# Kernel optimization log

Measured on AMD Instinct MI355X. Metric: run time of the kernel, lower is better.

Reference implementation:

```python
import jax, jax.numpy as jnp
import numpy as np

D = 256          # d_model
NH = 8           # n_heads
HD = D // NH
LEV = 3          # n_levels
NP = 4           # n_points
DFF = 1024       # d_ffn
B = 8            # batch
LQ = 3600        # 60*60 queries (hardcoded in get_reference_points)
SHAPES = np.array([[60, 60], [30, 30], [15, 15]], dtype=np.int64)
LIN = int((SHAPES[:, 0] * SHAPES[:, 1]).sum())  # 4725
START = np.concatenate([[0], np.cumsum(SHAPES[:, 0] * SHAPES[:, 1])[:-1]]).astype(np.int64)


def setup_inputs() -> dict:
    key = jax.random.key(0)
    ks = iter(jax.random.split(key, 32))
    def lin(k, o, i):
        return jax.random.normal(k, (o, i), jnp.float32) * 0.02
    return {
        "tgt": jax.random.normal(next(ks), (LQ, B, D), jnp.float32),
        "query_pos": jax.random.normal(next(ks), (1, 1, D), jnp.float32),
        "src": jax.random.normal(next(ks), (B, LIN, D), jnp.float32),
        "src_spatial_shapes": jnp.asarray(SHAPES),
        "level_start_index": jnp.asarray(START),
        "in_proj_w": lin(next(ks), 3 * D, D),
        "in_proj_b": jnp.zeros((3 * D,), jnp.float32),
        "out_proj_w": lin(next(ks), D, D),
        "out_proj_b": jnp.zeros((D,), jnp.float32),
        "samp_off_w": lin(next(ks), NH * LEV * NP * 2, D),
        "samp_off_b": jax.random.normal(next(ks), (NH * LEV * NP * 2,), jnp.float32) * 0.5,
        "attn_w_w": lin(next(ks), NH * LEV * NP, D),
        "attn_w_b": jnp.zeros((NH * LEV * NP,), jnp.float32),
        "value_proj_w": lin(next(ks), D, D),
        "value_proj_b": jnp.zeros((D,), jnp.float32),
        "cross_out_w": lin(next(ks), D, D),
        "cross_out_b": jnp.zeros((D,), jnp.float32),
        "ln1_g": jnp.ones((D,), jnp.float32), "ln1_b": jnp.zeros((D,), jnp.float32),
        "ln2_g": jnp.ones((D,), jnp.float32), "ln2_b": jnp.zeros((D,), jnp.float32),
        "ln3_g": jnp.ones((D,), jnp.float32), "ln3_b": jnp.zeros((D,), jnp.float32),
        "ffn_w1": lin(next(ks), DFF, D), "ffn_b1": jnp.zeros((DFF,), jnp.float32),
        "ffn_w2": lin(next(ks), D, DFF), "ffn_b2": jnp.zeros((D,), jnp.float32),
    }


def _ln(x, g, b, eps=1e-5):
    m = x.mean(-1, keepdims=True)
    v = ((x - m) ** 2).mean(-1, keepdims=True)
    return (x - m) * jax.lax.rsqrt(v + eps) * g + b


def _self_attn(q_in, k_in, v_in, wqkv, bqkv, wo, bo):
    # torch nn.MultiheadAttention semantics, inputs laid out (seq, batch, embed)
    S, N, _ = q_in.shape
    q = (q_in @ wqkv[:D].T + bqkv[:D]).reshape(S, N, NH, HD)
    k = (k_in @ wqkv[D:2 * D].T + bqkv[D:2 * D]).reshape(S, N, NH, HD)
    v = (v_in @ wqkv[2 * D:].T + bqkv[2 * D:]).reshape(S, N, NH, HD)
    logits = jnp.einsum('snhd,tnhd->nhst', q, k) / np.sqrt(HD).astype(np.float32)
    a = jax.nn.softmax(logits, -1)
    ctx = jnp.einsum('nhst,tnhd->snhd', a, v).reshape(S, N, D)
    return ctx @ wo.T + bo


def _bilinear(v_l, loc, Hl, Wl):
    # v_l: [B, NH, Hl*Wl, HD]; loc: [B, NH, LQ, NP, 2] normalized in [0,1]
    # grid_sample(align_corners=False, padding=zeros): pixel = loc*size - 0.5
    x = loc[..., 0] * Wl - 0.5
    y = loc[..., 1] * Hl - 0.5
    x0 = jnp.floor(x); y0 = jnp.floor(y)
    fx = x - x0; fy = y - y0
    x0 = x0.astype(jnp.int32); y0 = y0.astype(jnp.int32)
    def corner(yi, xi, w):
        valid = ((xi >= 0) & (xi < Wl) & (yi >= 0) & (yi < Hl)).astype(v_l.dtype)
        idx = jnp.clip(yi, 0, Hl - 1) * Wl + jnp.clip(xi, 0, Wl - 1)
        b, h, lq, p = idx.shape
        g = jnp.take_along_axis(v_l, idx.reshape(b, h, lq * p)[..., None], axis=2)
        return g.reshape(b, h, lq, p, HD) * (w * valid)[..., None]
    return (corner(y0, x0, (1 - fx) * (1 - fy))
            + corner(y0, x0 + 1, fx * (1 - fy))
            + corner(y0 + 1, x0, (1 - fx) * fy)
            + corner(y0 + 1, x0 + 1, fx * fy))


def _msdeform(query, ref, src, wso, bso, waw, baw, wv, bv, wo, bo):
    Bq, Lq, _ = query.shape
    value = (src @ wv.T + bv).reshape(Bq, LIN, NH, HD).transpose(0, 2, 1, 3)  # [B,NH,LIN,HD]
    off = (query @ wso.T + bso).reshape(Bq, Lq, NH, LEV, NP, 2)
    aw = (query @ waw.T + baw).reshape(Bq, Lq, NH, LEV * NP)
    aw = jax.nn.softmax(aw, -1).reshape(Bq, Lq, NH, LEV, NP)
    normalizer = jnp.asarray(SHAPES[:, ::-1].copy(), jnp.float32)  # (W, H) per level
    loc = ref[:, :, None, :, None, :] + off / normalizer[None, None, None, :, None, :]
    out = jnp.zeros((Bq, NH, Lq, HD), query.dtype)
    for l in range(LEV):
        Hl, Wl = int(SHAPES[l, 0]), int(SHAPES[l, 1])
        s = int(START[l])
        v_l = value[:, :, s:s + Hl * Wl]
        loc_l = loc[:, :, :, l].transpose(0, 2, 1, 3, 4)      # [B,NH,LQ,NP,2]
        sampled = _bilinear(v_l, loc_l, Hl, Wl)               # [B,NH,LQ,NP,HD]
        out = out + (sampled * aw[:, :, :, l].transpose(0, 2, 1, 3)[..., None]).sum(3)
    out = out.transpose(0, 2, 1, 3).reshape(Bq, Lq, D)
    return out @ wo.T + bo


def _reference_points():
    Hh = Ww = 60
    ys = (jnp.arange(Hh, dtype=jnp.float32) + 0.5) / Hh
    xs = (jnp.arange(Ww, dtype=jnp.float32) + 0.5) / Ww
    yy, xx = jnp.meshgrid(ys, xs, indexing='ij')
    ref = jnp.stack([xx.reshape(-1), yy.reshape(-1)], -1)[None]  # [1, 3600, 2]
    return jnp.broadcast_to(ref[:, :, None, :], (1, Hh * Ww, LEV, 2))


def reference(tgt, query_pos, src, src_spatial_shapes, level_start_index,
              in_proj_w, in_proj_b, out_proj_w, out_proj_b,
              samp_off_w, samp_off_b, attn_w_w, attn_w_b,
              value_proj_w, value_proj_b, cross_out_w, cross_out_b,
              ln1_g, ln1_b, ln2_g, ln2_b, ln3_g, ln3_b,
              ffn_w1, ffn_b1, ffn_w2, ffn_b2):
    # dropout layers are identity (eval mode). spatial shapes are static metadata
    # (SHAPES/START) since slicing sizes must be static under jit.
    q = (tgt + query_pos).transpose(1, 0, 2)
    tgt2 = _self_attn(q, q, tgt.transpose(1, 0, 2), in_proj_w, in_proj_b, out_proj_w, out_proj_b)
    t = _ln(tgt + tgt2.transpose(1, 0, 2), ln2_g, ln2_b)
    ref = _reference_points()
    tq = t.transpose(1, 0, 2)  # permute(1,0,2) -> [B, LQ, D]
    tgt2 = _msdeform(tq + query_pos, ref, src, samp_off_w, samp_off_b,
                     attn_w_w, attn_w_b, value_proj_w, value_proj_b,
                     cross_out_w, cross_out_b)
    tq = _ln(tq + tgt2, ln1_g, ln1_b)
    ff = jax.nn.relu(tq @ ffn_w1.T + ffn_b1) @ ffn_w2.T + ffn_b2
    tq = _ln(tq + ff, ln3_g, ln3_b)
    return tq.transpose(1, 0, 2)  # [LQ, B, D]
```

## Files before the change

kernel.cpp:

```cpp
#include <hip/hip_runtime.h>
#include <hip/hip_bf16.h>
#include <cstddef>
#include <cstdint>

#define D_MODEL 256
#define NHEAD   8
#define HDIM    32
#define NLEV    3
#define NPNT    4
#define DFF     1024
#define BATCH   8
#define LQ      3600
#define LIN     4725
#define MROWS   (BATCH*LQ)

typedef short bf16x8 __attribute__((ext_vector_type(8)));
typedef float f32x4  __attribute__((ext_vector_type(4)));

__device__ __forceinline__ unsigned short f2b(float x) {
    unsigned int u = __float_as_uint(x);
    unsigned int r = (u + 0x7fffu + ((u >> 16) & 1u)) >> 16;
    return (unsigned short)r;
}
__device__ __forceinline__ float b2f(unsigned short s) {
    return __uint_as_float(((unsigned int)s) << 16);
}

#define GLDS16(g, l) __builtin_amdgcn_global_load_lds( \
    (const __attribute__((address_space(1))) void*)(g), \
    (__attribute__((address_space(3))) void*)(l), 16, 0, 0)

#define WTOT 991232
__global__ __launch_bounds__(256) void prep_kernel(
    const float* __restrict__ tgt, unsigned short* __restrict__ tgtb,
    const float* __restrict__ srcf, unsigned short* __restrict__ srcb,
    const float* __restrict__ w_in, const float* __restrict__ w_out,
    const float* __restrict__ w_val, const float* __restrict__ w_cross,
    const float* __restrict__ w_so, const float* __restrict__ w_aw,
    const float* __restrict__ w_f1, const float* __restrict__ w_f2,
    unsigned short* __restrict__ wdst,
    const float* __restrict__ qp, const float* __restrict__ so_b,
    const float* __restrict__ aw_b, float* __restrict__ qpv)
{
    const int bid = blockIdx.x;
    const int tid = threadIdx.x;
    if (bid < 7200) {
        int i = bid * 256 + tid;
        float4 v = ((const float4*)tgt)[i];
        ushort4 o; o.x = f2b(v.x); o.y = f2b(v.y); o.z = f2b(v.z); o.w = f2b(v.w);
        ((ushort4*)tgtb)[i] = o;
    } else if (bid < 16650) {
        int i = (bid - 7200) * 256 + tid;
        float4 v = ((const float4*)srcf)[i];
        ushort4 o; o.x = f2b(v.x); o.y = f2b(v.y); o.z = f2b(v.z); o.w = f2b(v.w);
        ((ushort4*)srcb)[i] = o;
    } else if (bid < 17618) {
        int idx = ((bid - 16650) * 256 + tid) * 4;
        if (idx >= WTOT) return;
        const float* src; int off;
        if      (idx < 196608) { src = w_in;    off = idx; }
        else if (idx < 262144) { src = w_out;   off = idx - 196608; }
        else if (idx < 327680) { src = w_val;   off = idx - 262144; }
        else if (idx < 393216) { src = w_cross; off = idx - 327680; }
        else if (idx < 442368) { src = w_so;    off = idx - 393216; }
        else if (idx < 466944) { src = w_aw;    off = idx - 442368; }
        else if (idx < 729088) { src = w_f1;    off = idx - 466944; }
        else                   { src = w_f2;    off = idx - 729088; }
        float4 v = *(const float4*)(src + off);
        ushort4 o; o.x = f2b(v.x); o.y = f2b(v.y); o.z = f2b(v.z); o.w = f2b(v.w);
        *(ushort4*)(wdst + idx) = o;
    } else {
        int o = (bid - 17618) * 256 + tid;
        if (o >= 768 + 192 + 96) return;
        const float* wrow;
        if (o < 768)       wrow = w_in + (size_t)o * D_MODEL;
        else if (o < 960)  wrow = w_so + (size_t)(o - 768) * D_MODEL;
        else               wrow = w_aw + (size_t)(o - 960) * D_MODEL;
        float acc = 0.f;
        for (int d = 0; d < D_MODEL; ++d) acc += qp[d] * wrow[d];
        qpv[o] = acc;
        if (o >= 768) {
            float bias = (o < 960) ? so_b[o - 768] : aw_b[o - 960];
            qpv[1056 + (o - 768)] = acc + bias;
        }
    }
}

__global__ __launch_bounds__(256) void gemm_bf16(
    const unsigned short* __restrict__ A,
    const unsigned short* __restrict__ W,
    const float* __restrict__ bias,
    const float* __restrict__ bias2, int b2lim,
    float* __restrict__ Cf, unsigned short* __restrict__ Cb,
    int M, int N, int K, int relu)
{
    __shared__ __align__(16) unsigned short As[2 * 128 * 32];
    __shared__ __align__(16) unsigned short Bs[2 * 128 * 32];
    const int tid  = threadIdx.x;
    const int wave = tid >> 6;
    const int lane = tid & 63;
    const int m0 = blockIdx.x * 128;
    const int n0 = blockIdx.y * 128;

    const int lr  = lane >> 2;
    const int lc8 = (lane & 3) * 8;
    int ar0 = m0 + wave * 32 + lr;      if (ar0 > M - 1) ar0 = M - 1;
    int ar1 = m0 + wave * 32 + 16 + lr; if (ar1 > M - 1) ar1 = M - 1;
    int br0 = n0 + wave * 32 + lr;      if (br0 > N - 1) br0 = N - 1;
    int br1 = n0 + wave * 32 + 16 + lr; if (br1 > N - 1) br1 = N - 1;
    const unsigned short* pa0 = A + (size_t)ar0 * K + lc8;
    const unsigned short* pa1 = A + (size_t)ar1 * K + lc8;
    const unsigned short* pb0 = W + (size_t)br0 * K + lc8;
    const unsigned short* pb1 = W + (size_t)br1 * K + lc8;
    unsigned short* la0 = As + wave * 1024;
    unsigned short* la1 = As + wave * 1024 + 512;
    unsigned short* lb0 = Bs + wave * 1024;
    unsigned short* lb1 = Bs + wave * 1024 + 512;

    const int wm = (wave >> 1) * 64;
    const int wn = (wave & 1) * 64;
    const int fr = lane & 15;
    const int fk = (lane >> 4) * 8;

    f32x4 acc[4][4] = {};

    for (int k0 = 0; k0 < K; k0 += 64) {
        GLDS16(pa0, la0); GLDS16(pa0 + 32, la0 + 4096);
        GLDS16(pa1, la1); GLDS16(pa1 + 32, la1 + 4096);
        GLDS16(pb0, lb0); GLDS16(pb0 + 32, lb0 + 4096);
        GLDS16(pb1, lb1); GLDS16(pb1 + 32, lb1 + 4096);
        pa0 += 64; pa1 += 64; pb0 += 64; pb1 += 64;
        __syncthreads();
#pragma unroll
        for (int p = 0; p < 2; ++p) {
            bf16x8 af[4], bfv[4];
#pragma unroll
            for (int i = 0; i < 4; ++i)
                af[i] = *(const bf16x8*)&As[p * 4096 + (wm + i * 16 + fr) * 32 + fk];
#pragma unroll
            for (int j = 0; j < 4; ++j)
                bfv[j] = *(const bf16x8*)&Bs[p * 4096 + (wn + j * 16 + fr) * 32 + fk];
#pragma unroll
            for (int i = 0; i < 4; ++i)
#pragma unroll
                for (int j = 0; j < 4; ++j)
                    acc[i][j] = __builtin_amdgcn_mfma_f32_16x16x32_bf16(
                        af[i], bfv[j], acc[i][j], 0, 0, 0);
        }
        __syncthreads();
    }

    const int quad = lane >> 4;
#pragma unroll
    for (int j = 0; j < 4; ++j) {
        const int col = n0 + wn + j * 16 + fr;
        if (col >= N) continue;
        float bv = 0.f;
        if (bias) bv += bias[col];
        if (bias2 && col < b2lim) bv += bias2[col];
#pragma unroll
        for (int i = 0; i < 4; ++i) {
#pragma unroll
            for (int r = 0; r < 4; ++r) {
                const int row = m0 + wm + i * 16 + quad * 4 + r;
                if (row >= M) continue;
                float v = acc[i][j][r] + bv;
                if (relu) v = fmaxf(v, 0.f);
                if (Cf) Cf[(size_t)row * N + col] = v;
                if (Cb) Cb[(size_t)row * N + col] = f2b(v);
            }
        }
    }
}

__global__ __launch_bounds__(256) void gemm_ln(
    const unsigned short* __restrict__ A,
    const unsigned short* __restrict__ W,
    const float* __restrict__ bias,
    const float* __restrict__ resid,
    const float* __restrict__ g, const float* __restrict__ bb,
    float* __restrict__ outf, unsigned short* __restrict__ outb, int K)
{
    __shared__ __align__(16) unsigned short As[2 * 64 * 32];
    __shared__ __align__(16) unsigned short Bs[2 * 256 * 32];
    const int tid  = threadIdx.x;
    const int wave = tid >> 6;
    const int lane = tid & 63;
    const int m0 = blockIdx.x * 64;

    const int arow = tid >> 2;
    const int akc  = (tid & 3) * 8;
    const unsigned short* pa = A + (size_t)(m0 + arow) * K + akc;
    unsigned short* la = As + tid * 8;
    const unsigned short* pb0 = W + (size_t)(arow)       * K + akc;
    const unsigned short* pb1 = W + (size_t)(64  + arow) * K + akc;
    const unsigned short* pb2 = W + (size_t)(128 + arow) * K + akc;
    const unsigned short* pb3 = W + (size_t)(192 + arow) * K + akc;
    unsigned short* lb0 = Bs + tid * 8;
    unsigned short* lb1 = Bs + 2048 + tid * 8;
    unsigned short* lb2 = Bs + 4096 + tid * 8;
    unsigned short* lb3 = Bs + 6144 + tid * 8;

    const int fr = lane & 15;
    const int fk = (lane >> 4) * 8;
    const int quad = lane >> 4;
    const int colbase = wave * 64;

    f32x4 acc[4][4] = {};

    for (int k0 = 0; k0 < K; k0 += 64) {
        GLDS16(pa, la);        GLDS16(pa + 32, la + 2048);
        GLDS16(pb0, lb0);      GLDS16(pb0 + 32, lb0 + 8192);
        GLDS16(pb1, lb1);      GLDS16(pb1 + 32, lb1 + 8192);
        GLDS16(pb2, lb2);      GLDS16(pb2 + 32, lb2 + 8192);
        GLDS16(pb3, lb3);      GLDS16(pb3 + 32, lb3 + 8192);
        pa += 64; pb0 += 64; pb1 += 64; pb2 += 64; pb3 += 64;
        __syncthreads();
#pragma unroll
        for (int p = 0; p < 2; ++p) {
            bf16x8 af[4], bfv[4];
#pragma unroll
            for (int i = 0; i < 4; ++i)
                af[i] = *(const bf16x8*)&As[p * 2048 + (i * 16 + fr) * 32 + fk];
#pragma unroll
            for (int j = 0; j < 4; ++j)
                bfv[j] = *(const bf16x8*)&Bs[p * 8192 + (colbase + j * 16 + fr) * 32 + fk];
#pragma unroll
            for (int i = 0; i < 4; ++i)
#pragma unroll
                for (int j = 0; j < 4; ++j)
                    acc[i][j] = __builtin_amdgcn_mfma_f32_16x16x32_bf16(
                        af[i], bfv[j], acc[i][j], 0, 0, 0);
        }
        __syncthreads();
    }

    float2* red = (float2*)As;
    float rs[4][4], rq[4][4];
#pragma unroll
    for (int i = 0; i < 4; ++i) {
#pragma unroll
        for (int r = 0; r < 4; ++r) {
            const int row = m0 + i * 16 + quad * 4 + r;
            float s = 0.f, q = 0.f;
#pragma unroll
            for (int j = 0; j < 4; ++j) {
                const int col = colbase + j * 16 + fr;
                float v = acc[i][j][r] + bias[col] + resid[(size_t)row * 256 + col];
                acc[i][j][r] = v;
                s += v; q += v * v;
            }
            rs[i][r] = s; rq[i][r] = q;
        }
    }
#pragma unroll
    for (int off = 1; off < 16; off <<= 1) {
#pragma unroll
        for (int i = 0; i < 4; ++i)
#pragma unroll
            for (int r = 0; r < 4; ++r) {
                rs[i][r] += __shfl_xor(rs[i][r], off);
                rq[i][r] += __shfl_xor(rq[i][r], off);
            }
    }
    if ((lane & 15) == 0) {
#pragma unroll
        for (int i = 0; i < 4; ++i)
#pragma unroll
            for (int r = 0; r < 4; ++r)
                red[wave * 64 + i * 16 + quad * 4 + r] = make_float2(rs[i][r], rq[i][r]);
    }
    __syncthreads();
#pragma unroll
    for (int i = 0; i < 4; ++i) {
#pragma unroll
        for (int r = 0; r < 4; ++r) {
            const int rl = i * 16 + quad * 4 + r;
            const float2 t0 = red[rl], t1 = red[64 + rl], t2 = red[128 + rl], t3 = red[192 + rl];
            const float sum = t0.x + t1.x + t2.x + t3.x;
            const float sq  = t0.y + t1.y + t2.y + t3.y;
            const float mean = sum * (1.f / 256.f);
            const float var  = sq * (1.f / 256.f) - mean * mean;
            const float inv  = rsqrtf(var + 1e-5f);
            const int row = m0 + rl;
#pragma unroll
            for (int j = 0; j < 4; ++j) {
                const int col = colbase + j * 16 + fr;
                const float val = (acc[i][j][r] - mean) * inv * g[col] + bb[col];
                outf[(size_t)row * 256 + col] = val;
                if (outb) outb[(size_t)row * 256 + col] = f2b(val);
            }
        }
    }
}

__global__ __launch_bounds__(256) void ffn_fused_kernel(
    const unsigned short* __restrict__ A,
    const unsigned short* __restrict__ W1,
    const float* __restrict__ b1,
    const unsigned short* __restrict__ W2,
    const float* __restrict__ b2,
    const float* __restrict__ resid,
    const float* __restrict__ g, const float* __restrict__ bb,
    float* __restrict__ outf)
{
    __shared__ __align__(16) unsigned short Wc[16384];
    __shared__ __align__(16) unsigned short hid[2304];
    const int tid  = threadIdx.x;
    const int wave = tid >> 6;
    const int lane = tid & 63;
    const int m0 = blockIdx.x * 32;
    const int fr   = lane & 15;
    const int quad = lane >> 4;
    const int xm   = fr & 7;

#pragma unroll
    for (int j = 0; j < 4; ++j) {
        const int c  = wave * 4 + j;
        const int rA = c * 2 + (lane >> 5);
        const int k8 = (lane & 31) ^ (rA & 7);
        GLDS16(A + (size_t)(m0 + rA) * 256 + k8 * 8, Wc + c * 512);
    }
    int w1off[8], w2off[8];
#pragma unroll
    for (int j = 0; j < 8; ++j) {
        const int c  = wave * 8 + j;
        const int n1 = c * 2 + (lane >> 5);
        const int k1 = (lane & 31) ^ (n1 & 7);
        w1off[j] = n1 * 256 + k1 * 8;
        const int n2 = c * 8 + (lane >> 3);
        const int k2 = (lane & 7) ^ (n2 & 7);
        w2off[j] = n2 * 1024 + k2 * 8;
    }
    __syncthreads();
    bf16x8 af[2][8];
#pragma unroll
    for (int i = 0; i < 2; ++i)
#pragma unroll
        for (int s = 0; s < 8; ++s)
            af[i][s] = *(const bf16x8*)&Wc[((i * 16 + fr) * 32 + ((s * 4 + quad) ^ xm)) * 8];

    f32x4 acc2[2][4] = {};

    for (int h = 0; h < 16; ++h) {
        __syncthreads();
#pragma unroll
        for (int j = 0; j < 8; ++j)
            GLDS16(W1 + (size_t)h * 16384 + w1off[j], Wc + (wave * 8 + j) * 512);
        __syncthreads();
        f32x4 acc1[2] = {};
#pragma unroll
        for (int s = 0; s < 8; ++s) {
            bf16x8 bv = *(const bf16x8*)&Wc[((wave * 16 + fr) * 32 + ((s * 4 + quad) ^ xm)) * 8];
            acc1[0] = __builtin_amdgcn_mfma_f32_16x16x32_bf16(af[0][s], bv, acc1[0], 0, 0, 0);
            acc1[1] = __builtin_amdgcn_mfma_f32_16x16x32_bf16(af[1][s], bv, acc1[1], 0, 0, 0);
        }
        const float bias1 = b1[h * 64 + wave * 16 + fr];
#pragma unroll
        for (int i = 0; i < 2; ++i)
#pragma unroll
            for (int r = 0; r < 4; ++r) {
                float v = fmaxf(acc1[i][r] + bias1, 0.f);
                hid[(i * 16 + quad * 4 + r) * 72 + wave * 16 + fr] = f2b(v);
            }
        __syncthreads();
#pragma unroll
        for (int j = 0; j < 8; ++j)
            GLDS16(W2 + (size_t)h * 64 + w2off[j], Wc + (wave * 8 + j) * 512);
        __syncthreads();
#pragma unroll
        for (int s = 0; s < 2; ++s) {
            bf16x8 a2[2], b2v[4];
#pragma unroll
            for (int i = 0; i < 2; ++i)
                a2[i] = *(const bf16x8*)&hid[(i * 16 + fr) * 72 + s * 32 + quad * 8];
#pragma unroll
            for (int j2 = 0; j2 < 4; ++j2) {
                const int nb = wave * 64 + j2 * 16 + fr;
                b2v[j2] = *(const bf16x8*)&Wc[(nb * 8 + ((s * 4 + quad) ^ xm)) * 8];
            }
#pragma unroll
            for (int i = 0; i < 2; ++i)
#pragma unroll
                for (int j2 = 0; j2 < 4; ++j2)
                    acc2[i][j2] = __builtin_amdgcn_mfma_f32_16x16x32_bf16(
                        a2[i], b2v[j2], acc2[i][j2], 0, 0, 0);
        }
    }

    __syncthreads();
    float2* red = (float2*)hid;
    const int colbase = wave * 64;
    float rs[2][4], rq[2][4];
#pragma unroll
    for (int x = 0; x < 2; ++x) {
#pragma unroll
        for (int r = 0; r < 4; ++r) {
            const int row = m0 + x * 16 + quad * 4 + r;
            float s = 0.f, q = 0.f;
#pragma unroll
            for (int y = 0; y < 4; ++y) {
                const int col = colbase + y * 16 + fr;
                float v = acc2[x][y][r] + b2[col] + resid[(size_t)row * 256 + col];
                acc2[x][y][r] = v;
                s += v; q += v * v;
            }
            rs[x][r] = s; rq[x][r] = q;
        }
    }
#pragma unroll
    for (int off = 1; off < 16; off <<= 1) {
#pragma unroll
        for (int x = 0; x < 2; ++x)
#pragma unroll
            for (int r = 0; r < 4; ++r) {
                rs[x][r] += __shfl_xor(rs[x][r], off);
                rq[x][r] += __shfl_xor(rq[x][r], off);
            }
    }
    if ((lane & 15) == 0) {
#pragma unroll
        for (int x = 0; x < 2; ++x)
#pragma unroll
            for (int r = 0; r < 4; ++r)
                red[wave * 32 + x * 16 + quad * 4 + r] = make_float2(rs[x][r], rq[x][r]);
    }
    __syncthreads();
#pragma unroll
    for (int x = 0; x < 2; ++x) {
#pragma unroll
        for (int r = 0; r < 4; ++r) {
            const int rl = x * 16 + quad * 4 + r;
            const float2 t0 = red[rl], t1 = red[32 + rl], t2 = red[64 + rl], t3 = red[96 + rl];
            const float sum = t0.x + t1.x + t2.x + t3.x;
            const float sq  = t0.y + t1.y + t2.y + t3.y;
            const float mean = sum * (1.f / 256.f);
            const float var  = sq * (1.f / 256.f) - mean * mean;
            const float inv  = rsqrtf(var + 1e-5f);
            const int row = m0 + rl;
#pragma unroll
            for (int y = 0; y < 4; ++y) {
                const int col = colbase + y * 16 + fr;
                outf[(size_t)row * 256 + col] = (acc2[x][y][r] - mean) * inv * g[col] + bb[col];
            }
        }
    }
}

__global__ __launch_bounds__(256) void self_attn_kernel(
    const unsigned short* __restrict__ qkv, unsigned short* __restrict__ ctx)
{
    __shared__ float sh[8][768];
    __shared__ float ls[8][8][8];
    const int n = blockIdx.x;
    const int t = threadIdx.x;
#pragma unroll
    for (int s = 0; s < 8; ++s) {
        const unsigned short* row = qkv + (size_t)(n * 8 + s) * 768;
        sh[s][t]       = b2f(row[t]);
        sh[s][t + 256] = b2f(row[t + 256]);
        sh[s][t + 512] = b2f(row[t + 512]);
    }
    __syncthreads();
    const int h = t >> 5, j = t & 31;
#pragma unroll
    for (int pair = j; pair < 64; pair += 32) {
        const int s = pair >> 3, tt = pair & 7;
        float acc = 0.f;
#pragma unroll
        for (int d = 0; d < 32; ++d)
            acc += sh[s][h * 32 + d] * sh[tt][256 + h * 32 + d];
        ls[h][s][tt] = acc * 0.17677669529663687f;
    }
    __syncthreads();
    if (t < 64) {
        const int hh = t >> 3, s = t & 7;
        float mx = -1e30f;
        for (int tt = 0; tt < 8; ++tt) mx = fmaxf(mx, ls[hh][s][tt]);
        float sum = 0.f;
        for (int tt = 0; tt < 8; ++tt) { float e = expf(ls[hh][s][tt] - mx); ls[hh][s][tt] = e; sum += e; }
        const float inv = 1.f / sum;
        for (int tt = 0; tt < 8; ++tt) ls[hh][s][tt] *= inv;
    }
    __syncthreads();
#pragma unroll
    for (int s = 0; s < 8; ++s) {
        float acc = 0.f;
#pragma unroll
        for (int tt = 0; tt < 8; ++tt)
            acc += ls[h][s][tt] * sh[tt][512 + h * 32 + j];
        ctx[(size_t)(n * 8 + s) * D_MODEL + h * 32 + j] = f2b(acc);
    }
}

__global__ __launch_bounds__(256) void msdeform_kernel(
    const unsigned short* __restrict__ value,
    const float* __restrict__ comb,
    unsigned short* __restrict__ out)
{
    const int bid = blockIdx.x;
    const int b   = bid & 7;
    const int lq0 = (bid >> 3) * 4;
    const int r    = threadIdx.x >> 6;
    const int lane = threadIdx.x & 63;
    const int h = lane >> 3;
    const int l = lane & 7;
    const int lq = lq0 + r;
    const int m = lq * 8 + b;

    const float* offp = comb + (size_t)m * 288 + h * 24;
    const float* awp  = comb + (size_t)m * 288 + 192 + h * 12;
    float off[24], aw[12];
#pragma unroll
    for (int i = 0; i < 6; ++i) *(float4*)&off[i * 4] = ((const float4*)offp)[i];
#pragma unroll
    for (int i = 0; i < 3; ++i) *(float4*)&aw[i * 4] = ((const float4*)awp)[i];

    float mx = aw[0];
#pragma unroll
    for (int i = 1; i < 12; ++i) mx = fmaxf(mx, aw[i]);
    float se = 0.f;
#pragma unroll
    for (int i = 0; i < 12; ++i) { aw[i] = __expf(aw[i] - mx); se += aw[i]; }
    const float inv = 1.f / se;

    const float refx = ((lq % 60) + 0.5f) * (1.f / 60.f);
    const float refy = ((lq / 60) + 0.5f) * (1.f / 60.f);
    const int HW[3] = {60, 30, 15};
    const int ST[3] = {0, 3600, 4500};

    const unsigned short* vbase = value + (size_t)b * LIN * 256 + h * 32 + l * 4;

    float a0 = 0.f, a1 = 0.f, a2 = 0.f, a3 = 0.f;
#pragma unroll
    for (int lev = 0; lev < NLEV; ++lev) {
        const int Wl = HW[lev], s0 = ST[lev];
        const float fWl = (float)Wl;
#pragma unroll
        for (int p = 0; p < NPNT; ++p) {
            const int pt = lev * 4 + p;
            const float ox = off[lev * 8 + p * 2];
            const float oy = off[lev * 8 + p * 2 + 1];
            const float px = refx * fWl + ox - 0.5f;
            const float py = refy * fWl + oy - 0.5f;
            const float x0f = floorf(px), y0f = floorf(py);
            const float fx = px - x0f, fy = py - y0f;
            const int x0 = (int)x0f, y0 = (int)y0f;
            const float aww = aw[pt] * inv;
            const float vx0 = (x0 >= 0 && x0 < Wl) ? 1.f : 0.f;
            const float vx1 = (x0 >= -1 && x0 < Wl - 1) ? 1.f : 0.f;
            const float vy0 = (y0 >= 0 && y0 < Wl) ? 1.f : 0.f;
            const float vy1 = (y0 >= -1 && y0 < Wl - 1) ? 1.f : 0.f;
            const int xc0 = min(max(x0, 0), Wl - 1);
            const int xc1 = min(max(x0 + 1, 0), Wl - 1);
            const int yc0 = min(max(y0, 0), Wl - 1);
            const int yc1 = min(max(y0 + 1, 0), Wl - 1);
            const int sx  = xc1 - xc0;
            const int syW = (yc1 - yc0) * Wl;
            const int i00 = s0 + yc0 * Wl + xc0;
            const float w00 = (1.f - fx) * (1.f - fy) * aww * vx0 * vy0;
            const float w01 = fx * (1.f - fy) * aww * vx1 * vy0;
            const float w10 = (1.f - fx) * fy * aww * vx0 * vy1;
            const float w11 = fx * fy * aww * vx1 * vy1;
            const int i01 = i00 + sx;
            const int i10 = i00 + syW;
            const int i11 = i10 + sx;
            const ushort4 g00 = *(const ushort4*)(vbase + (size_t)i00 * 256);
            const ushort4 g01 = *(const ushort4*)(vbase + (size_t)i01 * 256);
            const ushort4 g10 = *(const ushort4*)(vbase + (size_t)i10 * 256);
            const ushort4 g11 = *(const ushort4*)(vbase + (size_t)i11 * 256);
            a0 += b2f(g00.x) * w00 + b2f(g01.x) * w01 + b2f(g10.x) * w10 + b2f(g11.x) * w11;
            a1 += b2f(g00.y) * w00 + b2f(g01.y) * w01 + b2f(g10.y) * w10 + b2f(g11.y) * w11;
            a2 += b2f(g00.z) * w00 + b2f(g01.z) * w01 + b2f(g10.z) * w10 + b2f(g11.z) * w11;
            a3 += b2f(g00.w) * w00 + b2f(g01.w) * w01 + b2f(g10.w) * w10 + b2f(g11.w) * w11;
        }
    }
    ushort4 o;
    o.x = f2b(a0); o.y = f2b(a1); o.z = f2b(a2); o.w = f2b(a3);
    *(ushort4*)(out + (size_t)m * 256 + h * 32 + l * 4) = o;
}

extern "C" void kernel_launch(void* const* d_in, const int* in_sizes, int n_in,
                              void* d_out, int out_size, void* d_ws, size_t ws_size,
                              hipStream_t stream)
{
    (void)in_sizes; (void)n_in; (void)out_size; (void)ws_size;
    const float* tgt          = (const float*)d_in[0];
    const float* qp           = (const float*)d_in[1];
    const float* src          = (const float*)d_in[2];
    const float* in_proj_w    = (const float*)d_in[5];
    const float* in_proj_b    = (const float*)d_in[6];
    const float* out_proj_w   = (const float*)d_in[7];
    const float* out_proj_b   = (const float*)d_in[8];
    const float* samp_off_w   = (const float*)d_in[9];
    const float* samp_off_b   = (const float*)d_in[10];
    const float* attn_w_w     = (const float*)d_in[11];
    const float* attn_w_b     = (const float*)d_in[12];
    const float* value_proj_w = (const float*)d_in[13];
    const float* value_proj_b = (const float*)d_in[14];
    const float* cross_out_w  = (const float*)d_in[15];
    const float* cross_out_b  = (const float*)d_in[16];
    const float* ln1_g = (const float*)d_in[17];
    const float* ln1_b = (const float*)d_in[18];
    const float* ln2_g = (const float*)d_in[19];
    const float* ln2_b = (const float*)d_in[20];
    const float* ln3_g = (const float*)d_in[21];
    const float* ln3_b = (const float*)d_in[22];
    const float* ffn_w1 = (const float*)d_in[23];
    const float* ffn_b1 = (const float*)d_in[24];
    const float* ffn_w2 = (const float*)d_in[25];
    const float* ffn_b2 = (const float*)d_in[26];
    float* out = (float*)d_out;

    float* ws    = (float*)d_ws;
    float* t     = ws;
    float* t2    = ws + 7372800;
    float* comb  = ws + 14745600;
    float* qpv   = ws + 23040000;
    float* cbias = qpv + 1056;

    unsigned short* bws    = (unsigned short*)((char*)d_ws + 92165376);
    unsigned short* s1     = bws;
    unsigned short* tgtb   = s1;
    unsigned short* ctxb   = s1;
    unsigned short* tb     = s1;
    unsigned short* t2b    = s1;
    unsigned short* s2     = bws + 7372800;
    unsigned short* qkvb   = s2;
    unsigned short* valueb = s2;
    unsigned short* msoutb = s2 + 9676800;
    unsigned short* srcb   = bws + 36864000;
    unsigned short* wtsb   = bws + 46540800;

    prep_kernel<<<17623, 256, 0, stream>>>(tgt, tgtb, src, srcb,
                                           in_proj_w, out_proj_w, value_proj_w,
                                           cross_out_w, samp_off_w, attn_w_w,
                                           ffn_w1, ffn_w2, wtsb,
                                           qp, samp_off_b, attn_w_b, qpv);
    gemm_bf16<<<dim3(225, 6), 256, 0, stream>>>(tgtb, wtsb + 0, in_proj_b, qpv, 512,
                                                nullptr, qkvb, MROWS, 768, 256, 0);
    self_attn_kernel<<<3600, 256, 0, stream>>>(qkvb, ctxb);
    gemm_ln<<<450, 256, 0, stream>>>(ctxb, wtsb + 196608, out_proj_b, tgt,
                                     ln2_g, ln2_b, t, tb, 256);
    gemm_bf16<<<dim3(296, 2), 256, 0, stream>>>(srcb, wtsb + 262144, value_proj_b, nullptr, 0,
                                                nullptr, valueb, BATCH * LIN, 256, 256, 0);
    gemm_bf16<<<dim3(225, 3), 256, 0, stream>>>(tb, wtsb + 393216, cbias, nullptr, 0,
                                                comb, nullptr, MROWS, 288, 256, 0);
    msdeform_kernel<<<7200, 256, 0, stream>>>(valueb, comb, msoutb);
    gemm_ln<<<450, 256, 0, stream>>>(msoutb, wtsb + 327680, cross_out_b, t,
                                     ln1_g, ln1_b, t2, t2b, 256);
    ffn_fused_kernel<<<900, 256, 0, stream>>>(t2b, wtsb + 466944, ffn_b1,
                                              wtsb + 729088, ffn_b2, t2,
                                              ln3_g, ln3_b, out);
}
```

Before: 453.0 us.

## Fuse cross-attention output projection and LayerNorm into the FFN kernel

Moves the cross-attention output GEMM, residual add and LN1 into the start of the fused FFN kernel. The normalized bf16 row tile goes straight into shared memory as the FFN input, so the separate gemm_ln launch and the bf16 round trip of t2b through global memory are gone. Costs: fp32 t2 is still written and then read back as the FFN residual, and the projection weights are reloaded per 32-row block across 900 blocks instead of 450 larger ones. The extra accumulator registers may also lower occupancy.

```diff
diff --git a/kernel.cpp b/kernel.cpp
--- a/kernel.cpp
+++ b/kernel.cpp
@@ -294,14 +294,18 @@
     }
 }
 
-__global__ __launch_bounds__(256) void ffn_fused_kernel(
+__global__ __launch_bounds__(256) void cross_ffn_kernel(
     const unsigned short* __restrict__ A,
+    const unsigned short* __restrict__ Wcr,
+    const float* __restrict__ bcr,
+    const float* __restrict__ resid1,
+    const float* __restrict__ g1, const float* __restrict__ b1g,
+    float* __restrict__ t2,
     const unsigned short* __restrict__ W1,
     const float* __restrict__ b1,
     const unsigned short* __restrict__ W2,
     const float* __restrict__ b2,
-    const float* __restrict__ resid,
-    const float* __restrict__ g, const float* __restrict__ bb,
+    const float* __restrict__ g3, const float* __restrict__ b3g,
     float* __restrict__ outf)
 {
     __shared__ __align__(16) unsigned short Wc[16384];
@@ -313,6 +317,7 @@
     const int fr   = lane & 15;
     const int quad = lane >> 4;
     const int xm   = fr & 7;
+    float2* red = (float2*)hid;
 
 #pragma unroll
     for (int j = 0; j < 4; ++j) {
@@ -340,6 +345,85 @@
         for (int s = 0; s < 8; ++s)
             af[i][s] = *(const bf16x8*)&Wc[((i * 16 + fr) * 32 + ((s * 4 + quad) ^ xm)) * 8];
 
+    f32x4 accc[4][2] = {};
+    for (int c = 0; c < 4; ++c) {
+        __syncthreads();
+#pragma unroll
+        for (int j = 0; j < 8; ++j)
+            GLDS16(Wcr + (size_t)c * 16384 + w1off[j], Wc + (wave * 8 + j) * 512);
+        __syncthreads();
+#pragma unroll
+        for (int s = 0; s < 8; ++s) {
+            bf16x8 bv = *(const bf16x8*)&Wc[((wave * 16 + fr) * 32 + ((s * 4 + quad) ^ xm)) * 8];
+            accc[c][0] = __builtin_amdgcn_mfma_f32_16x16x32_bf16(af[0][s], bv, accc[c][0], 0, 0, 0);
+            accc[c][1] = __builtin_amdgcn_mfma_f32_16x16x32_bf16(af[1][s], bv, accc[c][1], 0, 0, 0);
+        }
+    }
+
+    float rs[2][4], rq[2][4];
+#pragma unroll
+    for (int x = 0; x < 2; ++x) {
+#pragma unroll
+        for (int r = 0; r < 4; ++r) {
+            const int row = m0 + x * 16 + quad * 4 + r;
+            float s = 0.f, q = 0.f;
+#pragma unroll
+            for (int c = 0; c < 4; ++c) {
+                const int col = c * 64 + wave * 16 + fr;
+                float v = accc[c][x][r] + bcr[col] + resid1[(size_t)row * 256 + col];
+                accc[c][x][r] = v;
+                s += v; q += v * v;
+            }
+            rs[x][r] = s; rq[x][r] = q;
+        }
+    }
+#pragma unroll
+    for (int off = 1; off < 16; off <<= 1) {
+#pragma unroll
+        for (int x = 0; x < 2; ++x)
+#pragma unroll
+            for (int r = 0; r < 4; ++r) {
+                rs[x][r] += __shfl_xor(rs[x][r], off);
+                rq[x][r] += __shfl_xor(rq[x][r], off);
+            }
+    }
+    if ((lane & 15) == 0) {
+#pragma unroll
+        for (int x = 0; x < 2; ++x)
+#pragma unroll
+            for (int r = 0; r < 4; ++r)
+                red[wave * 32 + x * 16 + quad * 4 + r] = make_float2(rs[x][r], rq[x][r]);
+    }
+    __syncthreads();
+#pragma unroll
+    for (int x = 0; x < 2; ++x) {
+#pragma unroll
+        for (int r = 0; r < 4; ++r) {
+            const int rl = x * 16 + quad * 4 + r;
+            const float2 t0 = red[rl], t1 = red[32 + rl], t2r = red[64 + rl], t3 = red[96 + rl];
+            const float sum = t0.x + t1.x + t2r.x + t3.x;
+            const float sq  = t0.y + t1.y + t2r.y + t3.y;
+            const float mean = sum * (1.f / 256.f);
+            const float var  = sq * (1.f / 256.f) - mean * mean;
+            const float inv  = rsqrtf(var + 1e-5f);
+            const int row = m0 + rl;
+#pragma unroll
+            for (int c = 0; c < 4; ++c) {
+                const int col = c * 64 + wave * 16 + fr;
+                const float val = (accc[c][x][r] - mean) * inv * g1[col] + b1g[col];
+                t2[(size_t)row * 256 + col] = val;
+                const int g8 = col >> 3;
+                Wc[rl * 256 + ((g8 ^ (rl & 7)) << 3) + (col & 7)] = f2b(val);
+            }
+        }
+    }
+    __syncthreads();
+#pragma unroll
+    for (int i = 0; i < 2; ++i)
+#pragma unroll
+        for (int s = 0; s < 8; ++s)
+            af[i][s] = *(const bf16x8*)&Wc[((i * 16 + fr) * 32 + ((s * 4 + quad) ^ xm)) * 8];
+
     f32x4 acc2[2][4] = {};
 
     for (int h = 0; h < 16; ++h) {
@@ -389,9 +473,7 @@
     }
 
     __syncthreads();
-    float2* red = (float2*)hid;
     const int colbase = wave * 64;
-    float rs[2][4], rq[2][4];
 #pragma unroll
     for (int x = 0; x < 2; ++x) {
 #pragma unroll
@@ -401,7 +483,7 @@
 #pragma unroll
             for (int y = 0; y < 4; ++y) {
                 const int col = colbase + y * 16 + fr;
-                float v = acc2[x][y][r] + b2[col] + resid[(size_t)row * 256 + col];
+                float v = acc2[x][y][r] + b2[col] + t2[(size_t)row * 256 + col];
                 acc2[x][y][r] = v;
                 s += v; q += v * v;
             }
@@ -431,9 +513,9 @@
 #pragma unroll
         for (int r = 0; r < 4; ++r) {
             const int rl = x * 16 + quad * 4 + r;
-            const float2 t0 = red[rl], t1 = red[32 + rl], t2 = red[64 + rl], t3 = red[96 + rl];
-            const float sum = t0.x + t1.x + t2.x + t3.x;
-            const float sq  = t0.y + t1.y + t2.y + t3.y;
+            const float2 t0 = red[rl], t1 = red[32 + rl], t2r = red[64 + rl], t3 = red[96 + rl];
+            const float sum = t0.x + t1.x + t2r.x + t3.x;
+            const float sq  = t0.y + t1.y + t2r.y + t3.y;
             const float mean = sum * (1.f / 256.f);
             const float var  = sq * (1.f / 256.f) - mean * mean;
             const float inv  = rsqrtf(var + 1e-5f);
@@ -441,7 +523,7 @@
 #pragma unroll
             for (int y = 0; y < 4; ++y) {
                 const int col = colbase + y * 16 + fr;
-                outf[(size_t)row * 256 + col] = (acc2[x][y][r] - mean) * inv * g[col] + bb[col];
+                outf[(size_t)row * 256 + col] = (acc2[x][y][r] - mean) * inv * g3[col] + b3g[col];
             }
         }
     }
@@ -624,7 +706,6 @@
     unsigned short* tgtb   = s1;
     unsigned short* ctxb   = s1;
     unsigned short* tb     = s1;
-    unsigned short* t2b    = s1;
     unsigned short* s2     = bws + 7372800;
     unsigned short* qkvb   = s2;
     unsigned short* valueb = s2;
@@ -647,9 +728,9 @@
     gemm_bf16<<<dim3(225, 3), 256, 0, stream>>>(tb, wtsb + 393216, cbias, nullptr, 0,
                                                 comb, nullptr, MROWS, 288, 256, 0);
     msdeform_kernel<<<7200, 256, 0, stream>>>(valueb, comb, msoutb);
-    gemm_ln<<<450, 256, 0, stream>>>(msoutb, wtsb + 327680, cross_out_b, t,
-                                     ln1_g, ln1_b, t2, t2b, 256);
-    ffn_fused_kernel<<<900, 256, 0, stream>>>(t2b, wtsb + 466944, ffn_b1,
-                                              wtsb + 729088, ffn_b2, t2,
+    cross_ffn_kernel<<<900, 256, 0, stream>>>(msoutb, wtsb + 327680, cross_out_b,
+                                              t, ln1_g, ln1_b, t2,
+                                              wtsb + 466944, ffn_b1,
+                                              wtsb + 729088, ffn_b2,
                                               ln3_g, ln3_b, out);
 }
```

Result: no change. 452.9 us (-0.0%).
